# Kernel optimization log

Hardware: AMD Instinct MI355X
Metric: run time of the kernel (lower is better)

The kernel has to match this reference:

```python
import jax, jax.numpy as jnp
import numpy as np

B, S, D, E, K = 4, 4096, 4096, 64, 2
TEMP = 1.0  # temperature=1.0 -> scale by 1/temperature kept for faithfulness


def setup_inputs() -> dict:
    key = jax.random.key(0)
    k1, k2 = jax.random.split(key)
    x = jax.random.normal(k1, (B, S, D), dtype=jnp.float32)
    W_gate = jax.random.normal(k2, (E, D), dtype=jnp.float32) * (D ** -0.5)
    return {"x": x, "W_gate": W_gate}


def reference(x, W_gate):
    # gate: Linear(d_model, n_experts, bias=False) -> logits [B,S,E]
    logits = jnp.einsum('bsd,ed->bse', x, W_gate)
    # temperature scaling (eval mode: no jitter / expert dropout / gumbel)
    logits = logits * (1.0 / TEMP)
    probs_full = jax.nn.softmax(logits, axis=-1)           # [B,S,E]
    topk_vals, idx = jax.lax.top_k(logits, K)              # [B,S,K]
    scores = jax.nn.softmax(topk_vals, axis=-1)            # renormalized top-k gates
    # z-loss: mean(logsumexp(logits)^2)
    z = jax.nn.logsumexp(logits, axis=-1)                  # [B,S]
    z_loss = jnp.mean(z * z)
    # aux stats (computed under no_grad in the original)
    importance = jax.lax.stop_gradient(jnp.mean(probs_full, axis=(0, 1)))  # [E]
    idx_flat = idx.reshape(-1)
    counts = jnp.zeros((E,), probs_full.dtype).at[idx_flat].add(1.0)       # [E]
    load = jax.lax.stop_gradient(counts / jnp.maximum(jnp.sum(counts), 1.0))
    return (idx, scores, probs_full, z_loss, importance, load)
```

## Files before the change

kernel.cpp:

```cpp
#include <hip/hip_runtime.h>

namespace {
constexpr int D = 4096;
constexpr int E = 64;
constexpr int M = 16384;
constexpr int BM = 128;
constexpr int BK = 32;
constexpr int KSPLIT = 8;
constexpr int KC = D / KSPLIT;
constexpr int NT = KC / BK;
constexpr int ROWBLOCKS = M / BM;

constexpr int OFF_IDX = 0;
constexpr int OFF_SCORES = 32768;
constexpr int OFF_PROBS = 65536;
constexpr int OFF_Z = 1114112;
constexpr int OFF_IMP = 1114113;
constexpr int OFF_LOAD = 1114177;
}

__global__ __launch_bounds__(256, 4) void router_gemm(
    const float* __restrict__ xg, const float* __restrict__ wg,
    float* __restrict__ logits) {
  __shared__ __align__(16) float xs[BK][BM + 4];
  __shared__ __align__(16) float wsm[BK][E];

  const int t = threadIdx.x;
  const int bm = blockIdx.x & (ROWBLOCKS - 1);
  const int sp = blockIdx.x >> 7;
  const int row0 = bm * BM;
  const int k0 = sp * KC;

  const int tx = t & 15;
  const int ty = t >> 4;

  const int lrow = t >> 3;
  const int lcol = (t & 7) * 4;

  const float* xp = xg + (size_t)(row0 + lrow) * D + k0 + lcol;
  const float* wp = wg + (size_t)lrow * D + k0 + lcol;

  float4 xa[4];
  float4 wa[2];

  auto load_tile = [&](int kt) {
#pragma unroll
    for (int i = 0; i < 4; ++i)
      xa[i] = *(const float4*)(xp + (size_t)(i * 32) * D + kt);
#pragma unroll
    for (int i = 0; i < 2; ++i)
      wa[i] = *(const float4*)(wp + (size_t)(i * 32) * D + kt);
  };

  float acc[8][4];
#pragma unroll
  for (int i = 0; i < 8; ++i)
#pragma unroll
    for (int j = 0; j < 4; ++j) acc[i][j] = 0.f;

  load_tile(0);
  for (int tile = 0; tile < NT; ++tile) {
    __syncthreads();
#pragma unroll
    for (int i = 0; i < 4; ++i) {
      const int r = lrow + i * 32;
      xs[lcol + 0][r] = xa[i].x;
      xs[lcol + 1][r] = xa[i].y;
      xs[lcol + 2][r] = xa[i].z;
      xs[lcol + 3][r] = xa[i].w;
    }
#pragma unroll
    for (int i = 0; i < 2; ++i) {
      const int e = lrow + i * 32;
      wsm[lcol + 0][e] = wa[i].x;
      wsm[lcol + 1][e] = wa[i].y;
      wsm[lcol + 2][e] = wa[i].z;
      wsm[lcol + 3][e] = wa[i].w;
    }
    __syncthreads();
    if (tile + 1 < NT) load_tile((tile + 1) * BK);

    float4 a0 = *(const float4*)&xs[0][ty * 8];
    float4 a1 = *(const float4*)&xs[0][ty * 8 + 4];
    float4 b = *(const float4*)&wsm[0][tx * 4];
#pragma unroll
    for (int k = 0; k < BK; ++k) {
      float4 na0, na1, nb;
      if (k + 1 < BK) {
        na0 = *(const float4*)&xs[k + 1][ty * 8];
        na1 = *(const float4*)&xs[k + 1][ty * 8 + 4];
        nb = *(const float4*)&wsm[k + 1][tx * 4];
      }
      const float av[8] = {a0.x, a0.y, a0.z, a0.w, a1.x, a1.y, a1.z, a1.w};
      const float bv[4] = {b.x, b.y, b.z, b.w};
#pragma unroll
      for (int i = 0; i < 8; ++i)
#pragma unroll
        for (int j = 0; j < 4; ++j) acc[i][j] = fmaf(av[i], bv[j], acc[i][j]);
      if (k + 1 < BK) { a0 = na0; a1 = na1; b = nb; }
    }
  }

#pragma unroll
  for (int i = 0; i < 8; ++i) {
    const int r = row0 + ty * 8 + i;
#pragma unroll
    for (int j = 0; j < 4; ++j)
      atomicAdd(&logits[(size_t)r * E + tx * 4 + j], acc[i][j]);
  }
}

__global__ __launch_bounds__(64) void router_epilogue(
    const float* __restrict__ logits, float* __restrict__ out) {
  __shared__ float lds[64][65];
  __shared__ int cnt[64];

  const int l = threadIdx.x;
  const int r0 = blockIdx.x * 64;
  cnt[l] = 0;

#pragma unroll
  for (int rr = 0; rr < 16; ++rr) {
    const int row = rr * 4 + (l >> 4);
    const int c4 = (l & 15) * 4;
    const float4 v = *(const float4*)&logits[(size_t)(r0 + row) * 64 + c4];
    lds[row][c4 + 0] = v.x;
    lds[row][c4 + 1] = v.y;
    lds[row][c4 + 2] = v.z;
    lds[row][c4 + 3] = v.w;
  }
  __syncthreads();

  float v1 = -3.402823466e+38f, v2 = -3.402823466e+38f;
  int i1 = 0, i2 = 0;
#pragma unroll 8
  for (int e = 0; e < 64; ++e) {
    const float x = lds[l][e];
    if (x > v1) {
      v2 = v1; i2 = i1; v1 = x; i1 = e;
    } else if (x > v2) {
      v2 = x; i2 = e;
    }
  }

  float s = 0.f;
#pragma unroll 8
  for (int e = 0; e < 64; ++e) s += __expf(lds[l][e] - v1);
  const float z = v1 + __logf(s);
  const float rs = 1.f / s;

  const int r = r0 + l;
  out[OFF_IDX + 2 * r] = (float)i1;
  out[OFF_IDX + 2 * r + 1] = (float)i2;
  const float e1 = __expf(v2 - v1);
  const float s0 = 1.f / (1.f + e1);
  out[OFF_SCORES + 2 * r] = s0;
  out[OFF_SCORES + 2 * r + 1] = e1 * s0;
  atomicAdd(&cnt[i1], 1);
  atomicAdd(&cnt[i2], 1);

#pragma unroll 8
  for (int e = 0; e < 64; ++e) lds[l][e] = __expf(lds[l][e] - v1) * rs;
  __syncthreads();

#pragma unroll
  for (int rr = 0; rr < 16; ++rr) {
    const int row = rr * 4 + (l >> 4);
    const int c4 = (l & 15) * 4;
    float4 v;
    v.x = lds[row][c4 + 0];
    v.y = lds[row][c4 + 1];
    v.z = lds[row][c4 + 2];
    v.w = lds[row][c4 + 3];
    *(float4*)&out[OFF_PROBS + (size_t)(r0 + row) * 64 + c4] = v;
  }

  float ic = 0.f;
#pragma unroll 8
  for (int rr = 0; rr < 64; ++rr) ic += lds[rr][l];
  atomicAdd(&out[OFF_IMP + l], ic * (1.f / 16384.f));

  atomicAdd(&out[OFF_LOAD + l], (float)cnt[l] * (1.f / 32768.f));

  float zz = z * z;
#pragma unroll
  for (int off = 32; off > 0; off >>= 1) zz += __shfl_xor(zz, off);
  if (l == 0) atomicAdd(&out[OFF_Z], zz * (1.f / 16384.f) * (1.f / 64.f) * 64.f);
}

extern "C" void kernel_launch(void* const* d_in, const int* in_sizes, int n_in,
                              void* d_out, int out_size, void* d_ws, size_t ws_size,
                              hipStream_t stream) {
  const float* x = (const float*)d_in[0];
  const float* wgate = (const float*)d_in[1];
  float* out = (float*)d_out;
  float* logits = (float*)d_ws;

  hipMemsetAsync(logits, 0, (size_t)M * E * sizeof(float), stream);
  hipMemsetAsync(out + OFF_Z, 0, 129 * sizeof(float), stream);

  router_gemm<<<dim3(ROWBLOCKS * KSPLIT), dim3(256), 0, stream>>>(x, wgate, logits);
  router_epilogue<<<dim3(M / 64), dim3(64), 0, stream>>>(logits, out);
}
```

Baseline: 463.8 us.

## Fuse router GEMM with softmax/top-k epilogue using in-block split-K

Replaces the global split-K GEMM (atomic adds into a memset workspace) plus a separate epilogue kernel with one fused kernel. Each 512-thread block owns 64 rows over the full K and splits K four ways across thread groups, reducing partials through LDS. It then runs top-k, softmax and the z-loss in-block and writes per-block partial stats, which a tiny second kernel sums deterministically. The LDS tiles are double-buffered with an XOR swizzle. This removes the memsets, the global atomics and the logits round trip, but leaves only 256 blocks of 512 threads, so the GPU may be less fully occupied, and it adds in-block reduction syncs.

```diff
diff --git a/kernel.cpp b/kernel.cpp
--- a/kernel.cpp
+++ b/kernel.cpp
@@ -4,12 +4,10 @@
 constexpr int D = 4096;
 constexpr int E = 64;
 constexpr int M = 16384;
-constexpr int BM = 128;
-constexpr int BK = 32;
-constexpr int KSPLIT = 8;
-constexpr int KC = D / KSPLIT;
-constexpr int NT = KC / BK;
-constexpr int ROWBLOCKS = M / BM;
+constexpr int BM = 64;
+constexpr int BK = 64;
+constexpr int NT = D / BK;
+constexpr int NBLK = M / BM;
 
 constexpr int OFF_IDX = 0;
 constexpr int OFF_SCORES = 32768;
@@ -17,40 +15,53 @@
 constexpr int OFF_Z = 1114112;
 constexpr int OFF_IMP = 1114113;
 constexpr int OFF_LOAD = 1114177;
-}
-
-__global__ __launch_bounds__(256, 4) void router_gemm(
+
+constexpr int WS_STRIDE = 132;
+}
+
+__global__ __launch_bounds__(512, 2) void router_fused(
     const float* __restrict__ xg, const float* __restrict__ wg,
-    float* __restrict__ logits) {
-  __shared__ __align__(16) float xs[BK][BM + 4];
-  __shared__ __align__(16) float wsm[BK][E];
+    float* __restrict__ out, float* __restrict__ ws) {
+  __shared__ float smem[16384];
 
   const int t = threadIdx.x;
-  const int bm = blockIdx.x & (ROWBLOCKS - 1);
-  const int sp = blockIdx.x >> 7;
-  const int row0 = bm * BM;
-  const int k0 = sp * KC;
-
-  const int tx = t & 15;
-  const int ty = t >> 4;
-
-  const int lrow = t >> 3;
-  const int lcol = (t & 7) * 4;
-
-  const float* xp = xg + (size_t)(row0 + lrow) * D + k0 + lcol;
-  const float* wp = wg + (size_t)lrow * D + k0 + lcol;
-
-  float4 xa[4];
-  float4 wa[2];
-
-  auto load_tile = [&](int kt) {
-#pragma unroll
-    for (int i = 0; i < 4; ++i)
-      xa[i] = *(const float4*)(xp + (size_t)(i * 32) * D + kt);
-#pragma unroll
-    for (int i = 0; i < 2; ++i)
-      wa[i] = *(const float4*)(wp + (size_t)(i * 32) * D + kt);
+  const int u = t & 127;
+  const int s = t >> 7;
+  const int tx = u & 15;
+  const int ty = u >> 4;
+  const int r0 = blockIdx.x * BM;
+
+  const int sr = t >> 3;
+  const int sc = (t & 7) * 4;
+  const float* xp = xg + (size_t)(r0 + sr) * D + sc;
+  const float* wp = wg + (size_t)sr * D + sc;
+
+  float4 vx[2], vw[2];
+
+  auto stage_load = [&](int k0) {
+    vx[0] = *(const float4*)(xp + k0);
+    vx[1] = *(const float4*)(xp + k0 + 32);
+    vw[0] = *(const float4*)(wp + k0);
+    vw[1] = *(const float4*)(wp + k0 + 32);
   };
+  auto stage_write = [&](float* buf) {
+    float* Xs = buf;
+    float* Ws = buf + 4096;
+#pragma unroll
+    for (int h = 0; h < 2; ++h) {
+      const int c = sc + h * 32;
+      const int sw = ((c >> 4) & 3) << 3;
+      const int rp = sr ^ sw;
+      Xs[(c + 0) * 64 + rp] = vx[h].x;
+      Xs[(c + 1) * 64 + rp] = vx[h].y;
+      Xs[(c + 2) * 64 + rp] = vx[h].z;
+      Xs[(c + 3) * 64 + rp] = vx[h].w;
+      Ws[(c + 0) * 64 + rp] = vw[h].x;
+      Ws[(c + 1) * 64 + rp] = vw[h].y;
+      Ws[(c + 2) * 64 + rp] = vw[h].z;
+      Ws[(c + 3) * 64 + rp] = vw[h].w;
+    }
+  };
 
   float acc[8][4];
 #pragma unroll
@@ -58,134 +69,158 @@
 #pragma unroll
     for (int j = 0; j < 4; ++j) acc[i][j] = 0.f;
 
-  load_tile(0);
-  for (int tile = 0; tile < NT; ++tile) {
+  const int rbx = (ty * 8) ^ (s << 3);
+  const int rbw = (tx * 4) ^ (s << 3);
+
+  stage_load(0);
+  stage_write(smem);
+
+  for (int r = 0; r < NT; ++r) {
     __syncthreads();
-#pragma unroll
-    for (int i = 0; i < 4; ++i) {
-      const int r = lrow + i * 32;
-      xs[lcol + 0][r] = xa[i].x;
-      xs[lcol + 1][r] = xa[i].y;
-      xs[lcol + 2][r] = xa[i].z;
-      xs[lcol + 3][r] = xa[i].w;
+    if (r + 1 < NT) stage_load((r + 1) * BK);
+
+    const float* buf = smem + (r & 1) * 8192;
+    const float* Xs = buf + (size_t)(s * 16) * 64;
+    const float* Ws = buf + 4096 + (size_t)(s * 16) * 64;
+#pragma unroll
+    for (int kk = 0; kk < 16; ++kk) {
+      const float4 a0 = *(const float4*)&Xs[kk * 64 + rbx];
+      const float4 a1 = *(const float4*)&Xs[kk * 64 + rbx + 4];
+      const float4 bw = *(const float4*)&Ws[kk * 64 + rbw];
+      const float av[8] = {a0.x, a0.y, a0.z, a0.w, a1.x, a1.y, a1.z, a1.w};
+      const float bv[4] = {bw.x, bw.y, bw.z, bw.w};
+#pragma unroll
+      for (int i = 0; i < 8; ++i)
+#pragma unroll
+        for (int j = 0; j < 4; ++j) acc[i][j] = fmaf(av[i], bv[j], acc[i][j]);
     }
-#pragma unroll
-    for (int i = 0; i < 2; ++i) {
-      const int e = lrow + i * 32;
-      wsm[lcol + 0][e] = wa[i].x;
-      wsm[lcol + 1][e] = wa[i].y;
-      wsm[lcol + 2][e] = wa[i].z;
-      wsm[lcol + 3][e] = wa[i].w;
+    if (r + 1 < NT) stage_write(smem + ((r + 1) & 1) * 8192);
+  }
+
+  float* P = smem;
+  __syncthreads();
+  if (s >= 2) {
+    float* p = P + ((size_t)((s - 2) * 128 + u)) * 33;
+#pragma unroll
+    for (int i = 0; i < 8; ++i)
+#pragma unroll
+      for (int j = 0; j < 4; ++j) p[i * 4 + j] = acc[i][j];
+  }
+  __syncthreads();
+  if (s < 2) {
+    const float* p = P + ((size_t)(s * 128 + u)) * 33;
+#pragma unroll
+    for (int i = 0; i < 8; ++i)
+#pragma unroll
+      for (int j = 0; j < 4; ++j) acc[i][j] += p[i * 4 + j];
+  }
+  __syncthreads();
+  if (s == 1) {
+    float* p = P + (size_t)u * 33;
+#pragma unroll
+    for (int i = 0; i < 8; ++i)
+#pragma unroll
+      for (int j = 0; j < 4; ++j) p[i * 4 + j] = acc[i][j];
+  }
+  __syncthreads();
+
+  float* Lg = smem + 8448;
+  float* rowmax = smem + 12608;
+  float* rowrs = rowmax + 64;
+  float* zrow = rowrs + 64;
+  int* cnt = (int*)(zrow + 64);
+
+  if (s == 0) {
+    const float* p = P + (size_t)u * 33;
+#pragma unroll
+    for (int i = 0; i < 8; ++i)
+#pragma unroll
+      for (int j = 0; j < 4; ++j) {
+        const float v = acc[i][j] + p[i * 4 + j];
+        Lg[(ty * 8 + i) * 65 + tx * 4 + j] = v;
+      }
+  }
+  if (t < 64) cnt[t] = 0;
+  __syncthreads();
+
+  if (t < 64) {
+    const float* row = Lg + t * 65;
+    float v1 = -3.402823466e+38f, v2 = -3.402823466e+38f;
+    int i1 = 0, i2 = 0;
+#pragma unroll 8
+    for (int e = 0; e < 64; ++e) {
+      const float x = row[e];
+      if (x > v1) {
+        v2 = v1; i2 = i1; v1 = x; i1 = e;
+      } else if (x > v2) {
+        v2 = x; i2 = e;
+      }
     }
-    __syncthreads();
-    if (tile + 1 < NT) load_tile((tile + 1) * BK);
-
-    float4 a0 = *(const float4*)&xs[0][ty * 8];
-    float4 a1 = *(const float4*)&xs[0][ty * 8 + 4];
-    float4 b = *(const float4*)&wsm[0][tx * 4];
-#pragma unroll
-    for (int k = 0; k < BK; ++k) {
-      float4 na0, na1, nb;
-      if (k + 1 < BK) {
-        na0 = *(const float4*)&xs[k + 1][ty * 8];
-        na1 = *(const float4*)&xs[k + 1][ty * 8 + 4];
-        nb = *(const float4*)&wsm[k + 1][tx * 4];
-      }
-      const float av[8] = {a0.x, a0.y, a0.z, a0.w, a1.x, a1.y, a1.z, a1.w};
-      const float bv[4] = {b.x, b.y, b.z, b.w};
-#pragma unroll
-      for (int i = 0; i < 8; ++i)
-#pragma unroll
-        for (int j = 0; j < 4; ++j) acc[i][j] = fmaf(av[i], bv[j], acc[i][j]);
-      if (k + 1 < BK) { a0 = na0; a1 = na1; b = nb; }
-    }
-  }
-
-#pragma unroll
-  for (int i = 0; i < 8; ++i) {
-    const int r = row0 + ty * 8 + i;
-#pragma unroll
-    for (int j = 0; j < 4; ++j)
-      atomicAdd(&logits[(size_t)r * E + tx * 4 + j], acc[i][j]);
-  }
-}
-
-__global__ __launch_bounds__(64) void router_epilogue(
-    const float* __restrict__ logits, float* __restrict__ out) {
-  __shared__ float lds[64][65];
-  __shared__ int cnt[64];
-
-  const int l = threadIdx.x;
-  const int r0 = blockIdx.x * 64;
-  cnt[l] = 0;
-
-#pragma unroll
-  for (int rr = 0; rr < 16; ++rr) {
-    const int row = rr * 4 + (l >> 4);
-    const int c4 = (l & 15) * 4;
-    const float4 v = *(const float4*)&logits[(size_t)(r0 + row) * 64 + c4];
-    lds[row][c4 + 0] = v.x;
-    lds[row][c4 + 1] = v.y;
-    lds[row][c4 + 2] = v.z;
-    lds[row][c4 + 3] = v.w;
-  }
-  __syncthreads();
-
-  float v1 = -3.402823466e+38f, v2 = -3.402823466e+38f;
-  int i1 = 0, i2 = 0;
-#pragma unroll 8
-  for (int e = 0; e < 64; ++e) {
-    const float x = lds[l][e];
-    if (x > v1) {
-      v2 = v1; i2 = i1; v1 = x; i1 = e;
-    } else if (x > v2) {
-      v2 = x; i2 = e;
-    }
-  }
-
-  float s = 0.f;
-#pragma unroll 8
-  for (int e = 0; e < 64; ++e) s += __expf(lds[l][e] - v1);
-  const float z = v1 + __logf(s);
-  const float rs = 1.f / s;
-
-  const int r = r0 + l;
-  out[OFF_IDX + 2 * r] = (float)i1;
-  out[OFF_IDX + 2 * r + 1] = (float)i2;
-  const float e1 = __expf(v2 - v1);
-  const float s0 = 1.f / (1.f + e1);
-  out[OFF_SCORES + 2 * r] = s0;
-  out[OFF_SCORES + 2 * r + 1] = e1 * s0;
-  atomicAdd(&cnt[i1], 1);
-  atomicAdd(&cnt[i2], 1);
-
-#pragma unroll 8
-  for (int e = 0; e < 64; ++e) lds[l][e] = __expf(lds[l][e] - v1) * rs;
-  __syncthreads();
-
-#pragma unroll
-  for (int rr = 0; rr < 16; ++rr) {
-    const int row = rr * 4 + (l >> 4);
-    const int c4 = (l & 15) * 4;
-    float4 v;
-    v.x = lds[row][c4 + 0];
-    v.y = lds[row][c4 + 1];
-    v.z = lds[row][c4 + 2];
-    v.w = lds[row][c4 + 3];
-    *(float4*)&out[OFF_PROBS + (size_t)(r0 + row) * 64 + c4] = v;
-  }
-
-  float ic = 0.f;
-#pragma unroll 8
-  for (int rr = 0; rr < 64; ++rr) ic += lds[rr][l];
-  atomicAdd(&out[OFF_IMP + l], ic * (1.f / 16384.f));
-
-  atomicAdd(&out[OFF_LOAD + l], (float)cnt[l] * (1.f / 32768.f));
-
-  float zz = z * z;
-#pragma unroll
-  for (int off = 32; off > 0; off >>= 1) zz += __shfl_xor(zz, off);
-  if (l == 0) atomicAdd(&out[OFF_Z], zz * (1.f / 16384.f) * (1.f / 64.f) * 64.f);
+    float ssum = 0.f;
+#pragma unroll 8
+    for (int e = 0; e < 64; ++e) ssum += __expf(row[e] - v1);
+    const float z = v1 + __logf(ssum);
+    rowmax[t] = v1;
+    rowrs[t] = 1.f / ssum;
+    zrow[t] = z * z;
+
+    const int r = r0 + t;
+    out[OFF_IDX + 2 * r] = (float)i1;
+    out[OFF_IDX + 2 * r + 1] = (float)i2;
+    const float e1 = __expf(v2 - v1);
+    const float s0 = 1.f / (1.f + e1);
+    out[OFF_SCORES + 2 * r] = s0;
+    out[OFF_SCORES + 2 * r + 1] = e1 * s0;
+    atomicAdd(&cnt[i1], 1);
+    atomicAdd(&cnt[i2], 1);
+  }
+  __syncthreads();
+
+  {
+    const int pr = t >> 3;
+    const int pc = (t & 7) * 8;
+    float* prow = Lg + pr * 65 + pc;
+    const float m = rowmax[pr];
+    const float rs = rowrs[pr];
+    float p[8];
+#pragma unroll
+    for (int q = 0; q < 8; ++q) p[q] = __expf(prow[q] - m) * rs;
+    float4 o0 = {p[0], p[1], p[2], p[3]};
+    float4 o1 = {p[4], p[5], p[6], p[7]};
+    *(float4*)&out[OFF_PROBS + (size_t)(r0 + pr) * 64 + pc] = o0;
+    *(float4*)&out[OFF_PROBS + (size_t)(r0 + pr) * 64 + pc + 4] = o1;
+#pragma unroll
+    for (int q = 0; q < 8; ++q) prow[q] = p[q];
+  }
+  __syncthreads();
+
+  if (t < 64) {
+    float ic = 0.f;
+#pragma unroll 8
+    for (int rr = 0; rr < 64; ++rr) ic += Lg[rr * 65 + t];
+    ws[(size_t)blockIdx.x * WS_STRIDE + t] = ic;
+    ws[(size_t)blockIdx.x * WS_STRIDE + 64 + t] = (float)cnt[t];
+    float zz = zrow[t];
+#pragma unroll
+    for (int off = 32; off > 0; off >>= 1) zz += __shfl_xor(zz, off);
+    if (t == 0) ws[(size_t)blockIdx.x * WS_STRIDE + 128] = zz;
+  }
+}
+
+__global__ __launch_bounds__(192) void router_reduce(
+    const float* __restrict__ ws, float* __restrict__ out) {
+  const int t = threadIdx.x;
+  if (t < 129) {
+    float v = 0.f;
+#pragma unroll 8
+    for (int b = 0; b < NBLK; ++b) v += ws[(size_t)b * WS_STRIDE + t];
+    if (t < 64)
+      out[OFF_IMP + t] = v * (1.f / 16384.f);
+    else if (t < 128)
+      out[OFF_LOAD + (t - 64)] = v * (1.f / 32768.f);
+    else
+      out[OFF_Z] = v * (1.f / 16384.f);
+  }
 }
 
 extern "C" void kernel_launch(void* const* d_in, const int* in_sizes, int n_in,
@@ -194,11 +229,8 @@
   const float* x = (const float*)d_in[0];
   const float* wgate = (const float*)d_in[1];
   float* out = (float*)d_out;
-  float* logits = (float*)d_ws;
-
-  hipMemsetAsync(logits, 0, (size_t)M * E * sizeof(float), stream);
-  hipMemsetAsync(out + OFF_Z, 0, 129 * sizeof(float), stream);
-
-  router_gemm<<<dim3(ROWBLOCKS * KSPLIT), dim3(256), 0, stream>>>(x, wgate, logits);
-  router_epilogue<<<dim3(M / 64), dim3(64), 0, stream>>>(logits, out);
-}
+  float* ws = (float*)d_ws;
+
+  router_fused<<<dim3(NBLK), dim3(512), 0, stream>>>(x, wgate, out, ws);
+  router_reduce<<<dim3(1), dim3(192), 0, stream>>>(ws, out);
+}
```

After: 409.0 us. 11.8% less time.
